# Optimization experiments

Hardware: AMD Instinct MI355X
Metric: run time of the kernel (lower is better)

The kernel has to match this reference:

```python
import jax, jax.numpy as jnp
import numpy as np

PERIOD = 7   # statsmodels seasonal_decompose period used in season()
L_P = 16     # patch length hardcoded in patches()
STRIDE = 8   # stride hardcoded in patches()

B, C, L, D = 16, 64, 512, 768


def _decompose(x):
    """Vectorized additive seasonal_decompose (period=7) over last axis.

    Matches statsmodels: trend = centered 7-pt moving average (edges NaN in
    statsmodels; represented as 0 here so the math stays finite), seasonal =
    de-meaned per-phase average of the detrended interior, resid = x - trend
    - seasonal on the valid interior (0 at edges, where statsmodels has NaN).
    x: [B, C, L]
    """
    Lx = x.shape[-1]
    half = PERIOD // 2  # 3
    cs = jnp.concatenate([jnp.zeros(x.shape[:-1] + (1,), x.dtype), jnp.cumsum(x, -1)], -1)
    ma = (cs[..., PERIOD:] - cs[..., :-PERIOD]) / PERIOD  # [B,C,L-6] centers 3..L-4
    trend = jnp.zeros_like(x).at[..., half:Lx - half].set(ma)
    idx = jnp.arange(Lx)
    mask = (idx >= half) & (idx < Lx - half)          # valid interior
    ph = idx % PERIOD
    det = jnp.where(mask, x - trend, 0.0)             # detrended (0 where invalid)
    Pm = jax.nn.one_hot(ph, PERIOD, dtype=x.dtype) * mask[:, None].astype(x.dtype)  # [L,7]
    sums = jnp.einsum('bcl,lp->bcp', det, Pm)         # per-phase sums over valid idx
    counts = Pm.sum(0)                                # per-phase valid counts
    pavg = sums / counts
    pavg = pavg - pavg.mean(-1, keepdims=True)        # de-mean the 7 phase averages
    seasonal = jnp.take(pavg, ph, axis=-1)            # tile to [B,C,L]
    resid = jnp.where(mask, x - trend - seasonal, 0.0)
    return trend, seasonal, resid


def setup_inputs() -> dict:
    key = jax.random.key(0)
    ks = jax.random.split(key, 12)
    s = 0.02
    return {
        'data_x': jax.random.normal(ks[0], (B, C, L), jnp.float32),
        'data_y': jax.random.normal(ks[1], (B, C, L), jnp.float32),
        'gamma': jax.random.uniform(ks[2], (B, C, L), jnp.float32),
        'beta': jax.random.uniform(ks[3], (B, C, L), jnp.float32),
        'w_trend': jax.random.normal(ks[4], (L_P, L), jnp.float32) * s,
        'b_trend': jax.random.normal(ks[5], (L_P,), jnp.float32) * s,
        'w_seasonal': jax.random.normal(ks[6], (L_P, L), jnp.float32) * s,
        'b_seasonal': jax.random.normal(ks[7], (L_P,), jnp.float32) * s,
        'w_resid': jax.random.normal(ks[8], (L_P, L), jnp.float32) * s,
        'b_resid': jax.random.normal(ks[9], (L_P,), jnp.float32) * s,
        'w_g': jax.random.normal(ks[10], (D, 3 * L_P), jnp.float32) * s,
        'b_g': jax.random.normal(ks[11], (D,), jnp.float32) * s,
    }


def reference(data_x, data_y, gamma, beta, w_trend, b_trend, w_seasonal,
              b_seasonal, w_resid, b_resid, w_g, b_g):
    Lx = data_x.shape[-1]
    # transformed(): RevIN-like affine with mean/sqrt(var) (epsi=0, unbiased var)
    mean = data_x.mean(1)
    var = data_x.var(1, ddof=1)
    m = (mean / jnp.sqrt(var))[:, None, :]
    xt = gamma * (data_x - m) + beta
    # season() detaches its input in the original
    xt = jax.lax.stop_gradient(xt)
    trend, seasonal, resid = _decompose(xt)
    # patches(): per-stream Linear(L->16), concat, Linear(48->D)
    t = trend @ w_trend.T + b_trend          # [B,C,16]
    s = seasonal @ w_seasonal.T + b_seasonal
    r = resid @ w_resid.T + b_resid
    cat = jnp.concatenate([t, s, r], -1)     # [B,C,48]
    p = cat @ w_g.T + b_g                    # [B,C,D]
    # unsqueeze(2).expand(...) before cat -> every patch slot is identical
    N_p = int((Lx + L_P) / STRIDE + 2)
    return jnp.broadcast_to(p[:, :, None, :], p.shape[:2] + (N_p, p.shape[-1]))
```

## Files before the change

### kernel.cpp

```cpp
#include <hip/hip_runtime.h>

#define Bx 16
#define Cx 64
#define Lx 512
#define Dx 768
#define NPx 68
#define PER 7

__global__ void mean_var_kernel(const float* __restrict__ x,
                                float* __restrict__ m) {
    int idx = blockIdx.x * blockDim.x + threadIdx.x;
    if (idx >= Bx * Lx) return;
    int b = idx / Lx, l = idx - b * Lx;
    const float* xp = x + (size_t)b * Cx * Lx + l;
    float s = 0.f, ss = 0.f;
#pragma unroll 8
    for (int c = 0; c < Cx; ++c) {
        float v = xp[(size_t)c * Lx];
        s += v;
        ss += v * v;
    }
    float mean = s / (float)Cx;
    float var = (ss - s * s / (float)Cx) / (float)(Cx - 1);
    m[idx] = mean * rsqrtf(var);
}

__global__ __launch_bounds__(256) void token_kernel(
    const float* __restrict__ x, const float* __restrict__ gamma,
    const float* __restrict__ beta, const float* __restrict__ m,
    const float* __restrict__ w_t, const float* __restrict__ b_t,
    const float* __restrict__ w_s, const float* __restrict__ b_s,
    const float* __restrict__ w_r, const float* __restrict__ b_r,
    const float* __restrict__ w_g, const float* __restrict__ b_g,
    float* __restrict__ out) {
    __shared__ float s_xt[Lx];
    __shared__ float s_tr[Lx];
    __shared__ float s_se[Lx];
    __shared__ float s_res[Lx];
    __shared__ float s_ph[PER];
    __shared__ float s_cat[48];
    __shared__ float s_p[Dx];

    const int bc = blockIdx.x;
    const int b = bc / Cx;
    const int tid = threadIdx.x;

    const float* xp = x + (size_t)bc * Lx;
    const float* gp = gamma + (size_t)bc * Lx;
    const float* bp = beta + (size_t)bc * Lx;
    const float* mp = m + (size_t)b * Lx;

    for (int l = tid; l < Lx; l += 256)
        s_xt[l] = gp[l] * (xp[l] - mp[l]) + bp[l];
    __syncthreads();

    for (int l = tid; l < Lx; l += 256) {
        float t = 0.f;
        if (l >= 3 && l <= Lx - 4) {
#pragma unroll
            for (int k = -3; k <= 3; ++k) t += s_xt[l + k];
            t *= (1.f / 7.f);
        }
        s_tr[l] = t;
    }
    __syncthreads();

    if (tid < PER) {
        int p = tid;
        int l0 = p + 7 * ((3 - p + 6) / 7);
        float sum = 0.f;
        int cnt = 0;
        for (int l = l0; l <= Lx - 4; l += 7) {
            sum += s_xt[l] - s_tr[l];
            ++cnt;
        }
        s_ph[p] = sum / (float)cnt;
    }
    __syncthreads();
    if (tid == 0) {
        float mn = 0.f;
#pragma unroll
        for (int p = 0; p < PER; ++p) mn += s_ph[p];
        mn *= (1.f / 7.f);
#pragma unroll
        for (int p = 0; p < PER; ++p) s_ph[p] -= mn;
    }
    __syncthreads();

    for (int l = tid; l < Lx; l += 256) {
        float se = s_ph[l % PER];
        s_se[l] = se;
        s_res[l] = (l >= 3 && l <= Lx - 4) ? (s_xt[l] - s_tr[l] - se) : 0.f;
    }
    __syncthreads();

    {
        int j = tid >> 2, q = tid & 3;
        if (j < 48) {
            const float* stream;
            const float* w;
            const float* bias;
            int jj;
            if (j < 16) {
                stream = s_tr; w = w_t; bias = b_t; jj = j;
            } else if (j < 32) {
                stream = s_se; w = w_s; bias = b_s; jj = j - 16;
            } else {
                stream = s_res; w = w_r; bias = b_r; jj = j - 32;
            }
            const float* wr = w + (size_t)jj * Lx + q * 128;
            const float* sp = stream + q * 128;
            float acc = 0.f;
#pragma unroll 4
            for (int i = 0; i < 128; ++i) acc += sp[i] * wr[i];
            acc += __shfl_xor(acc, 1);
            acc += __shfl_xor(acc, 2);
            if (q == 0) s_cat[j] = acc + bias[jj];
        }
    }
    __syncthreads();

    for (int d = tid; d < Dx; d += 256) {
        const float4* wg4 = reinterpret_cast<const float4*>(w_g + (size_t)d * 48);
        const float4* c4 = reinterpret_cast<const float4*>(s_cat);
        float acc = 0.f;
#pragma unroll
        for (int kk = 0; kk < 12; ++kk) {
            float4 w4 = wg4[kk], cc = c4[kk];
            acc += w4.x * cc.x + w4.y * cc.y + w4.z * cc.z + w4.w * cc.w;
        }
        s_p[d] = acc + b_g[d];
    }
    __syncthreads();

    float4* outp = reinterpret_cast<float4*>(out + (size_t)bc * NPx * Dx);
    const float4* p4 = reinterpret_cast<const float4*>(s_p);
    const int nvec = NPx * (Dx / 4);
    for (int i = tid; i < nvec; i += 256) {
        outp[i] = p4[i % 192];
    }
}

extern "C" void kernel_launch(void* const* d_in, const int* in_sizes, int n_in,
                              void* d_out, int out_size, void* d_ws,
                              size_t ws_size, hipStream_t stream) {
    const float* data_x = (const float*)d_in[0];
    const float* gamma = (const float*)d_in[2];
    const float* beta = (const float*)d_in[3];
    const float* w_t = (const float*)d_in[4];
    const float* b_t = (const float*)d_in[5];
    const float* w_s = (const float*)d_in[6];
    const float* b_s = (const float*)d_in[7];
    const float* w_r = (const float*)d_in[8];
    const float* b_r = (const float*)d_in[9];
    const float* w_g = (const float*)d_in[10];
    const float* b_g = (const float*)d_in[11];
    float* out = (float*)d_out;
    float* m = (float*)d_ws;

    int nthreads_m = Bx * Lx;
    mean_var_kernel<<<(nthreads_m + 255) / 256, 256, 0, stream>>>(data_x, m);

    token_kernel<<<Bx * Cx, 256, 0, stream>>>(data_x, gamma, beta, m, w_t, b_t,
                                              w_s, b_s, w_r, b_r, w_g, b_g,
                                              out);
}
```

Baseline: 65.51 us.

## Split output broadcast into separate high-parallelism kernel and vectorize projection dots

The token kernel now writes only the first patch row of each output slice. A new broadcast kernel replicates that row into the remaining 67 slots, with more threads and blocks spread across chunks. The per-stream projection dot products use float4 loads. The aim is to spread the large store-bound broadcast over more waves, independent of the token kernel's shared-memory occupancy. In exchange it adds a kernel launch and a re-read of each first row.

```diff
diff --git a/kernel.cpp b/kernel.cpp
--- a/kernel.cpp
+++ b/kernel.cpp
@@ -33,13 +33,12 @@
     const float* __restrict__ w_r, const float* __restrict__ b_r,
     const float* __restrict__ w_g, const float* __restrict__ b_g,
     float* __restrict__ out) {
-    __shared__ float s_xt[Lx];
-    __shared__ float s_tr[Lx];
-    __shared__ float s_se[Lx];
-    __shared__ float s_res[Lx];
+    __shared__ __align__(16) float s_xt[Lx];
+    __shared__ __align__(16) float s_tr[Lx];
+    __shared__ __align__(16) float s_se[Lx];
+    __shared__ __align__(16) float s_res[Lx];
     __shared__ float s_ph[PER];
-    __shared__ float s_cat[48];
-    __shared__ float s_p[Dx];
+    __shared__ __align__(16) float s_cat[48];
 
     const int bc = blockIdx.x;
     const int b = bc / Cx;
@@ -108,11 +107,15 @@
             } else {
                 stream = s_res; w = w_r; bias = b_r; jj = j - 32;
             }
-            const float* wr = w + (size_t)jj * Lx + q * 128;
-            const float* sp = stream + q * 128;
+            const float4* wr =
+                reinterpret_cast<const float4*>(w + (size_t)jj * Lx + q * 128);
+            const float4* sp = reinterpret_cast<const float4*>(stream + q * 128);
             float acc = 0.f;
-#pragma unroll 4
-            for (int i = 0; i < 128; ++i) acc += sp[i] * wr[i];
+#pragma unroll
+            for (int i = 0; i < 32; ++i) {
+                float4 a = sp[i], wv = wr[i];
+                acc += a.x * wv.x + a.y * wv.y + a.z * wv.z + a.w * wv.w;
+            }
             acc += __shfl_xor(acc, 1);
             acc += __shfl_xor(acc, 2);
             if (q == 0) s_cat[j] = acc + bias[jj];
@@ -120,25 +123,34 @@
     }
     __syncthreads();
 
+    float* outp = out + (size_t)bc * NPx * Dx;
+    const float4* c4 = reinterpret_cast<const float4*>(s_cat);
     for (int d = tid; d < Dx; d += 256) {
         const float4* wg4 = reinterpret_cast<const float4*>(w_g + (size_t)d * 48);
-        const float4* c4 = reinterpret_cast<const float4*>(s_cat);
         float acc = 0.f;
 #pragma unroll
         for (int kk = 0; kk < 12; ++kk) {
             float4 w4 = wg4[kk], cc = c4[kk];
             acc += w4.x * cc.x + w4.y * cc.y + w4.z * cc.z + w4.w * cc.w;
         }
-        s_p[d] = acc + b_g[d];
+        outp[d] = acc + b_g[d];
     }
-    __syncthreads();
+}
 
-    float4* outp = reinterpret_cast<float4*>(out + (size_t)bc * NPx * Dx);
-    const float4* p4 = reinterpret_cast<const float4*>(s_p);
-    const int nvec = NPx * (Dx / 4);
-    for (int i = tid; i < nvec; i += 256) {
-        outp[i] = p4[i % 192];
-    }
+__global__ __launch_bounds__(256) void broadcast_kernel(float* __restrict__ out) {
+    int gid = blockIdx.x * 256 + threadIdx.x;
+    int d4 = gid % 192;
+    int tmp = gid / 192;
+    int bc = tmp & 1023;
+    int chunk = tmp >> 10;
+
+    float4* row = reinterpret_cast<float4*>(out) + (size_t)bc * (NPx * 192);
+    float4 v = row[d4];
+
+    int n0 = 1 + chunk * 17;
+    int cnt = min(17, NPx - n0);
+    float4* dst = row + (size_t)n0 * 192 + d4;
+    for (int n = 0; n < cnt; ++n) dst[n * 192] = v;
 }
 
 extern "C" void kernel_launch(void* const* d_in, const int* in_sizes, int n_in,
@@ -164,4 +176,6 @@
     token_kernel<<<Bx * Cx, 256, 0, stream>>>(data_x, gamma, beta, m, w_t, b_t,
                                               w_s, b_s, w_r, b_r, w_g, b_g,
                                               out);
+
+    broadcast_kernel<<<(4 * Bx * Cx * 192) / 256, 256, 0, stream>>>(out);
 }
```

Measured after the change: 69.75 us. 6.5% more time.
